# Kernel optimization log

Hardware: AMD Instinct MI355X
Metric: run time of the kernel (lower is better)

Reference implementation:

```python
import jax, jax.numpy as jnp
import numpy as np

N, E, D, H, C, G, L = 100000, 1600000, 128, 4, 32, 4096, 3  # nodes, edges, h_dim, heads, head_dim, graphs, conv blocks


def setup_inputs() -> dict:
    key = jax.random.key(0)
    ks = jax.random.split(key, 24)
    s = 0.05
    w = lambda k, shape: jax.random.normal(k, shape, jnp.float32) * s
    inp = {
        "x": jax.random.normal(ks[0], (N, D), jnp.float32),
        "edge_index": jax.random.randint(ks[1], (2, E), 0, N),
        "batch": jnp.sort(jax.random.randint(ks[2], (N,), 0, G)),
        # input TransformerConv (in=D, out=C per head, H heads, beta=True)
        "in_Wq": w(ks[3], (D, D)), "in_bq": jnp.zeros((D,), jnp.float32),
        "in_Wk": w(ks[4], (D, D)), "in_bk": jnp.zeros((D,), jnp.float32),
        "in_Wv": w(ks[5], (D, D)), "in_bv": jnp.zeros((D,), jnp.float32),
        "in_Ws": w(ks[6], (D, D)), "in_bs": jnp.zeros((D,), jnp.float32),
        "in_Wbeta": w(ks[7], (3 * D,)),
        # stacked conv blocks (L of them, in=out=D)
        "blk_Wq": w(ks[8], (L, D, D)), "blk_bq": jnp.zeros((L, D), jnp.float32),
        "blk_Wk": w(ks[9], (L, D, D)), "blk_bk": jnp.zeros((L, D), jnp.float32),
        "blk_Wv": w(ks[10], (L, D, D)), "blk_bv": jnp.zeros((L, D), jnp.float32),
        "blk_Ws": w(ks[11], (L, D, D)), "blk_bs": jnp.zeros((L, D), jnp.float32),
        "blk_Wbeta": w(ks[12], (L, 3 * D)),
        # MLP head
        "W1": w(ks[13], (D, 64)), "b1": jnp.zeros((64,), jnp.float32),
        "W2": w(ks[14], (64, 32)), "b2": jnp.zeros((32,), jnp.float32),
        "W3": w(ks[15], (32, 1)), "b3": jnp.zeros((1,), jnp.float32),
    }
    return inp


def transformer_conv(x, src, dst, Wq, bq, Wk, bk, Wv, bv, Ws, bs, Wbeta):
    # PyG TransformerConv, concat=True, root_weight=True, beta=True, eval mode
    q = (x @ Wq + bq).reshape(N, H, C)
    k = (x @ Wk + bk).reshape(N, H, C)
    v = (x @ Wv + bv).reshape(N, H, C)
    # per-edge attention logits: message j=src -> i=dst
    alpha = jnp.einsum("ehc,ehc->eh", q[dst], k[src]) / jnp.sqrt(jnp.float32(C))  # [E,H]
    m = jax.ops.segment_max(alpha, dst, num_segments=N)
    m = jnp.where(jnp.isfinite(m), m, 0.0)
    e = jnp.exp(alpha - m[dst])
    denom = jax.ops.segment_sum(e, dst, num_segments=N)
    a = e / (denom[dst] + 1e-16)  # segment softmax over in-edges of dst
    msg = a[..., None] * v[src]  # [E,H,C]
    out = jax.ops.segment_sum(msg, dst, num_segments=N).reshape(N, H * C)
    x_r = x @ Ws + bs
    beta = jax.nn.sigmoid(jnp.concatenate([out, x_r, out - x_r], axis=-1) @ Wbeta)[:, None]
    return beta * x_r + (1.0 - beta) * out


def reference(x, edge_index, batch, in_Wq, in_bq, in_Wk, in_bk, in_Wv, in_bv,
              in_Ws, in_bs, in_Wbeta, blk_Wq, blk_bq, blk_Wk, blk_bk, blk_Wv,
              blk_bv, blk_Ws, blk_bs, blk_Wbeta, W1, b1, W2, b2, W3, b3):
    src, dst = edge_index[0], edge_index[1]
    h = jax.nn.relu(transformer_conv(x, src, dst, in_Wq, in_bq, in_Wk, in_bk,
                                     in_Wv, in_bv, in_Ws, in_bs, in_Wbeta))
    for l in range(L):  # dropout is identity in eval mode
        h = jax.nn.relu(transformer_conv(h, src, dst, blk_Wq[l], blk_bq[l],
                                         blk_Wk[l], blk_bk[l], blk_Wv[l], blk_bv[l],
                                         blk_Ws[l], blk_bs[l], blk_Wbeta[l]))
    # global mean pool over graphs
    sums = jax.ops.segment_sum(h, batch, num_segments=G)
    cnt = jax.ops.segment_sum(jnp.ones((N, 1), h.dtype), batch, num_segments=G)
    g = sums / jnp.maximum(cnt, 1.0)
    g = jax.nn.relu(g @ W1 + b1)
    g = jax.nn.relu(g @ W2 + b2)
    return jax.nn.sigmoid(g @ W3 + b3)
```

## Files before the change

### kernel.cpp

```cpp
#include <hip/hip_runtime.h>
#include <hip/hip_bf16.h>
#include <cstdint>

#define DH 128
#define NB 256
#define NBK 1024

typedef __attribute__((ext_vector_type(8))) short short8;
typedef __attribute__((ext_vector_type(4))) float floatx4;
typedef __attribute__((ext_vector_type(2))) float floatx2;

__device__ __forceinline__ float bflo(unsigned u) { return __uint_as_float(u << 16); }
__device__ __forceinline__ float bfhi(unsigned u) { return __uint_as_float(u & 0xffff0000u); }

__device__ __forceinline__ unsigned pk_bf16(float a, float b) {
  return ((unsigned)__bfloat16_as_ushort(__float2bfloat16(b)) << 16)
       | (unsigned)__bfloat16_as_ushort(__float2bfloat16(a));
}

template<int CTRL>
__device__ __forceinline__ float dpp_add(float x) {
  int y = __builtin_amdgcn_update_dpp(0, __float_as_int(x), CTRL, 0xf, 0xf, true);
  return x + __int_as_float(y);
}


__global__ void cvt_bf16(const float* __restrict__ x, __hip_bfloat16* __restrict__ o, int n) {
  int i = blockIdx.x * 256 + threadIdx.x;
  if (i < n) o[i] = __float2bfloat16(x[i]);
}


__global__ void scan1_kernel(const int* __restrict__ deg, int* __restrict__ off,
                             int* __restrict__ bsum, int n) {
  __shared__ int sh[256];
  int idx = blockIdx.x * 256 + threadIdx.x;
  int v = (idx < n) ? deg[idx] : 0;
  sh[threadIdx.x] = v;
  __syncthreads();
  for (int d = 1; d < 256; d <<= 1) {
    int x = (threadIdx.x >= (unsigned)d) ? sh[threadIdx.x - d] : 0;
    __syncthreads();
    sh[threadIdx.x] += x;
    __syncthreads();
  }
  if (idx < n) off[idx] = sh[threadIdx.x] - v;
  if (threadIdx.x == 255) bsum[blockIdx.x] = sh[255];
}

__global__ void scan2_kernel(int* __restrict__ bsum, int nb) {
  __shared__ int sh[512];
  int t = threadIdx.x;
  int v = (t < nb) ? bsum[t] : 0;
  sh[t] = v;
  __syncthreads();
  for (int d = 1; d < 512; d <<= 1) {
    int x = (t >= (unsigned)d) ? sh[t - d] : 0;
    __syncthreads();
    sh[t] += x;
    __syncthreads();
  }
  if (t < nb) bsum[t] = sh[t] - v;
}

__global__ void scan3_kernel(int* __restrict__ off, const int* __restrict__ bsum, int n) {
  int idx = blockIdx.x * 256 + threadIdx.x;
  if (idx < n) off[idx] += bsum[blockIdx.x];
}


__global__ __launch_bounds__(256)
void csr_p1(const int* __restrict__ dst, int* __restrict__ hist, int E, int chunk) {
  __shared__ int cnt[NBK];
  const int blk = blockIdx.x, tid = threadIdx.x;
  for (int c = tid; c < NBK; c += 256) cnt[c] = 0;
  __syncthreads();
  int base = blk * chunk;
  int end = base + chunk; if (end > E) end = E;
  for (int e = base + tid; e < end; e += 256) atomicAdd(&cnt[dst[e] >> 7], 1);
  __syncthreads();
  for (int c = tid; c < NBK; c += 256) hist[c * NB + blk] = cnt[c];
}


__global__ __launch_bounds__(256)
void csr_p2(int* __restrict__ hist, int* __restrict__ total) {
  int b = blockIdx.x * 4 + (threadIdx.x >> 6);
  int lane = threadIdx.x & 63;
  int4 v = *(int4*)&hist[b * NB + lane * 4];
  int s0 = v.x;
  int s1 = s0 + v.y;
  int s2 = s1 + v.z;
  int s3 = s2 + v.w;
  int t = s3;
  for (int d = 1; d < 64; d <<= 1) {
    int y = __shfl_up(t, d);
    if (lane >= d) t += y;
  }
  int excl = t - s3;
  int4 o;
  o.x = excl; o.y = excl + s0; o.z = excl + s1; o.w = excl + s2;
  *(int4*)&hist[b * NB + lane * 4] = o;
  if (lane == 63) total[b] = t;
}

__global__ __launch_bounds__(256)
void csr_p3(const int* __restrict__ src, const int* __restrict__ dst,
            const int* __restrict__ hist, const int* __restrict__ tstart,
            int* __restrict__ part, int E, int chunk) {
  __shared__ int cur[NBK];
  const int blk = blockIdx.x, tid = threadIdx.x;
  for (int c = tid; c < NBK; c += 256) cur[c] = hist[c * NB + blk] + tstart[c];
  __syncthreads();
  int base = blk * chunk;
  int end = base + chunk; if (end > E) end = E;
  for (int e = base + tid; e < end; e += 256) {
    int d = dst[e];
    int b = d >> 7;
    int pos = atomicAdd(&cur[b], 1);
    part[pos] = (src[e] << 7) | (d & 127);
  }
}

__global__ __launch_bounds__(256)
void csr_p4(const int* __restrict__ part, const int* __restrict__ tstart,
            const int* __restrict__ total, int* __restrict__ deg,
            int* __restrict__ off, int* __restrict__ csr, int Nn) {
  __shared__ int lcnt[128], lscan[128], lcur[128];
  const int b = blockIdx.x, tid = threadIdx.x;
  const int p0 = tstart[b];
  const int m = total[b];
  if (tid < 128) lcnt[tid] = 0;
  __syncthreads();
  for (int k = tid; k < m; k += 256) atomicAdd(&lcnt[part[p0 + k] & 127], 1);
  __syncthreads();
  if (tid < 128) lscan[tid] = lcnt[tid];
  __syncthreads();
  for (int d = 1; d < 128; d <<= 1) {
    int v = 0;
    if (tid < 128 && tid >= d) v = lscan[tid - d];
    __syncthreads();
    if (tid < 128) lscan[tid] += v;
    __syncthreads();
  }
  if (tid < 128) {
    int ex = lscan[tid] - lcnt[tid];
    lcur[tid] = ex;
    int n = (b << 7) + tid;
    if (n < Nn) { deg[n] = lcnt[tid]; off[n] = p0 + ex; }
  }
  __syncthreads();
  for (int k = tid; k < m; k += 256) {
    int pk = part[p0 + k];
    int pos = p0 + atomicAdd(&lcur[pk & 127], 1);
    csr[pos] = pk >> 7;
  }
}


__global__ void goff_kernel(const int* __restrict__ batch, int* __restrict__ goff,
                            int N, int G) {
  int g = blockIdx.x * 256 + threadIdx.x;
  if (g > G) return;
  if (g == G) { goff[G] = N; return; }
  int lo = 0, hi = N;
  while (lo < hi) { int mid = (lo + hi) >> 1; if (batch[mid] < g) lo = mid + 1; else hi = mid; }
  goff[g] = lo;
}


__global__ __launch_bounds__(256)
void pack_w_kernel(const float* __restrict__ Wq, const float* __restrict__ Wk,
                   const float* __restrict__ Wv, const float* __restrict__ Ws,
                   const float* __restrict__ bq, const float* __restrict__ bk,
                   const float* __restrict__ bv, const float* __restrict__ bs,
                   __hip_bfloat16* __restrict__ WT2, float* __restrict__ bcat) {
  if (blockIdx.x == 64) {
    for (int c = threadIdx.x; c < 512; c += 256) {
      int which = c >> 7, cc = c & 127;
      const float* b = (which == 0) ? bq : (which == 1) ? bk : (which == 2) ? bv : bs;
      bcat[c] = b[cc];
    }
    return;
  }
  __shared__ float tile[32][33];
  const int bid = blockIdx.x;
  const int which = bid >> 4, kb = (bid >> 2) & 3, cb = bid & 3;
  const float* W = (which == 0) ? Wq : (which == 1) ? Wk : (which == 2) ? Wv : Ws;
  const int tx = threadIdx.x & 31, ty = threadIdx.x >> 5;
#pragma unroll
  for (int r = ty; r < 32; r += 8)
    tile[r][tx] = W[(kb * 32 + r) * 128 + cb * 32 + tx];
  __syncthreads();
  const int t = threadIdx.x;
  const int mt_sel = t >> 7;
  const int s4 = (t & 127) * 4;
  const int l16 = s4 >> 5;
  const int quad = (s4 >> 3) & 3;
  const int j0 = s4 & 7;
  const int cl = mt_sel * 16 + l16;
  const int kr = quad * 8 + j0;
  float f0 = tile[kr + 0][cl];
  float f1 = tile[kr + 1][cl];
  float f2 = tile[kr + 2][cl];
  float f3 = tile[kr + 3][cl];
  const int mt = which * 8 + cb * 2 + mt_sel;
  const int o = mt * 2048 + kb * 512 + l16 * 32 + quad * 8 + j0;
  uint2 w;
  w.x = pk_bf16(f0, f1);
  w.y = pk_bf16(f2, f3);
  *(uint2*)&((unsigned short*)WT2)[o] = w;
}


__global__ __launch_bounds__(256)
void gemm_qkvs(const short* __restrict__ Xb, const short* __restrict__ WT2,
               const float* __restrict__ bc,
               unsigned int* __restrict__ qout,
               unsigned int* __restrict__ kvp,
               unsigned int* __restrict__ xrout, int Nn) {
  __shared__ short As[64][132];
  const int row0 = blockIdx.x * 64;
  const int tid = threadIdx.x;

#pragma unroll
  for (int p = 0; p < 4; ++p) {
    int chunk = p * 256 + tid;
    int r = chunk >> 4, c8 = chunk & 15;
    int row = row0 + r; if (row >= Nn) row = Nn - 1;
    *(int4*)&As[r][c8 * 8] = *(const int4*)&Xb[(size_t)row * 128 + c8 * 8];
  }
  __syncthreads();

  const int w = tid >> 6, lane = tid & 63, quad = lane >> 4, l16 = lane & 15;

  short8 xf[4][4];
#pragma unroll
  for (int nt = 0; nt < 4; ++nt)
#pragma unroll
    for (int kt = 0; kt < 4; ++kt)
      xf[nt][kt] = *(const short8*)&As[nt * 16 + l16][kt * 32 + quad * 8];

  const int fbase = l16 * 32 + quad * 8;

  if (w == 0 || w == 3) {
    unsigned int* outp = (w == 0) ? qout : xrout;
    const int mbase = (w == 0) ? 0 : 24;
#pragma unroll
    for (int i = 0; i < 8; ++i) {
      const int mt = mbase + i;
      short8 af[4];
#pragma unroll
      for (int kt = 0; kt < 4; ++kt)
        af[kt] = *(const short8*)&WT2[mt * 2048 + kt * 512 + fbase];
      float4 bias = *(const float4*)&bc[mt * 16 + quad * 4];
      const int wc = (i * 16 + quad * 4);
#pragma unroll
      for (int nt = 0; nt < 4; ++nt) {
        floatx4 acc = (floatx4){0.f, 0.f, 0.f, 0.f};
#pragma unroll
        for (int kt = 0; kt < 4; ++kt)
          acc = __builtin_amdgcn_mfma_f32_16x16x32_bf16(af[kt], xf[nt][kt], acc, 0, 0, 0);
        int node = row0 + nt * 16 + l16;
        if (node < Nn) {
          uint2 o;
          o.x = pk_bf16(acc[0] + bias.x, acc[1] + bias.y);
          o.y = pk_bf16(acc[2] + bias.z, acc[3] + bias.w);
          *(uint2*)&outp[(size_t)node * 64 + (wc >> 1)] = o;
        }
      }
    }
  } else {
    const int kb = 8 + (w - 1) * 4;
    const int vb = 16 + (w - 1) * 4;
#pragma unroll
    for (int i = 0; i < 4; ++i) {
      const int mk = kb + i, mv = vb + i;
      short8 afk[4], afv[4];
#pragma unroll
      for (int kt = 0; kt < 4; ++kt) {
        afk[kt] = *(const short8*)&WT2[mk * 2048 + kt * 512 + fbase];
        afv[kt] = *(const short8*)&WT2[mv * 2048 + kt * 512 + fbase];
      }
      float4 bk4 = *(const float4*)&bc[mk * 16 + quad * 4];
      float4 bv4 = *(const float4*)&bc[mv * 16 + quad * 4];
      const int krel = (w - 1) * 64 + i * 16 + quad * 4;
#pragma unroll
      for (int nt = 0; nt < 4; ++nt) {
        floatx4 ak = (floatx4){0.f, 0.f, 0.f, 0.f};
        floatx4 av = (floatx4){0.f, 0.f, 0.f, 0.f};
#pragma unroll
        for (int kt = 0; kt < 4; ++kt) {
          ak = __builtin_amdgcn_mfma_f32_16x16x32_bf16(afk[kt], xf[nt][kt], ak, 0, 0, 0);
          av = __builtin_amdgcn_mfma_f32_16x16x32_bf16(afv[kt], xf[nt][kt], av, 0, 0, 0);
        }
        int node = row0 + nt * 16 + l16;
        if (node < Nn) {
          int d0 = __builtin_amdgcn_cvt_pk_fp8_f32(ak[0] + bk4.x, ak[1] + bk4.y, 0, false);
          d0 = __builtin_amdgcn_cvt_pk_fp8_f32(av[0] + bv4.x, av[1] + bv4.y, d0, true);
          int d1 = __builtin_amdgcn_cvt_pk_fp8_f32(ak[2] + bk4.z, ak[3] + bk4.w, 0, false);
          d1 = __builtin_amdgcn_cvt_pk_fp8_f32(av[2] + bv4.z, av[3] + bv4.w, d1, true);
          uint2 o; o.x = (unsigned)d0; o.y = (unsigned)d1;
          *(uint2*)&kvp[(size_t)node * 64 + (krel >> 1)] = o;
        }
      }
    }
  }
}


__global__ __launch_bounds__(256)
void attn_kernel(unsigned int* __restrict__ q_h, const unsigned int* __restrict__ kvp,
                 const unsigned int* __restrict__ xrb, const int* __restrict__ off,
                 const int* __restrict__ deg, const int* __restrict__ csr,
                 const float* __restrict__ Wb, int Nn) {
  int wv = __builtin_amdgcn_readfirstlane(threadIdx.x >> 6);
  int i = blockIdx.x * 4 + wv;
  if (i >= Nn) return;
  int l = threadIdx.x & 63;

  unsigned qp = q_h[(size_t)i * 64 + l];
  float q0 = bflo(qp), q1 = bfhi(qp);
  int e0 = off[i], e1 = e0 + deg[i];

  float den0 = 0.f, x00 = 0.f, x10 = 0.f;
  float den1 = 0.f, x01 = 0.f, x11 = 0.f;
  float den2 = 0.f, x02 = 0.f, x12 = 0.f;
  float den3 = 0.f, x03 = 0.f, x13 = 0.f;

  auto body = [&](int e, float& den, float& a0, float& a1) {
    int s = csr[e];
    int kq = (int)kvp[(s << 6) | l];
    floatx2 kk = __builtin_amdgcn_cvt_pk_f32_fp8(kq, false);
    floatx2 vv = __builtin_amdgcn_cvt_pk_f32_fp8(kq, true);
    float d = q0 * kk.x + q1 * kk.y;
    d = dpp_add<0x128>(d);
    d = dpp_add<0x124>(d);
    d = dpp_add<0x122>(d);
    d = dpp_add<0x121>(d);
    float p = __expf(d * 0.17677669529663687f);
    den += p; a0 += p * vv.x; a1 += p * vv.y;
  };

  int e = e0;
  for (; e + 3 < e1; e += 4) {
    body(e + 0, den0, x00, x10);
    body(e + 1, den1, x01, x11);
    body(e + 2, den2, x02, x12);
    body(e + 3, den3, x03, x13);
  }
  for (; e < e1; ++e) body(e, den0, x00, x10);

  float denom = den0 + den1 + den2 + den3 + 1e-16f;
  float o0 = (x00 + x01 + x02 + x03) / denom;
  float o1 = (x10 + x11 + x12 + x13) / denom;

  unsigned xp = xrb[(size_t)i * 64 + l];
  float xr0 = bflo(xp), xr1 = bfhi(xp);

  float c = o0 * Wb[2 * l] + o1 * Wb[2 * l + 1]
          + xr0 * Wb[128 + 2 * l] + xr1 * Wb[128 + 2 * l + 1]
          + (o0 - xr0) * Wb[256 + 2 * l] + (o1 - xr1) * Wb[256 + 2 * l + 1];
  c += __shfl_xor(c, 1);
  c += __shfl_xor(c, 2);
  c += __shfl_xor(c, 4);
  c += __shfl_xor(c, 8);
  c += __shfl_xor(c, 16);
  c += __shfl_xor(c, 32);
  float beta = 1.f / (1.f + __expf(-c));
  float h0 = fmaxf(beta * xr0 + (1.f - beta) * o0, 0.f);
  float h1 = fmaxf(beta * xr1 + (1.f - beta) * o1, 0.f);
  q_h[(size_t)i * 64 + l] = pk_bf16(h0, h1);
}


__global__ __launch_bounds__(128)
void poolmlp_kernel(const unsigned short* __restrict__ h, const int* __restrict__ goff,
                    const float* __restrict__ W1, const float* __restrict__ b1,
                    const float* __restrict__ W2, const float* __restrict__ b2,
                    const float* __restrict__ W3, const float* __restrict__ b3,
                    float* __restrict__ out) {
  int g = blockIdx.x;
  int t = threadIdx.x;
  int n0 = goff[g], cnt = goff[g + 1] - n0;
  float s = 0.f;
  for (int n = n0; n < n0 + cnt; ++n) s += bflo(h[(size_t)n * 128 + t]);
  __shared__ float gv[128];
  __shared__ float t1[64];
  __shared__ float t2[32];
  gv[t] = s / fmaxf((float)cnt, 1.0f);
  __syncthreads();
  if (t < 64) {
    float a = b1[t];
    for (int k = 0; k < 128; ++k) a += gv[k] * W1[k * 64 + t];
    t1[t] = fmaxf(a, 0.f);
  }
  __syncthreads();
  if (t < 32) {
    float a = b2[t];
    for (int k = 0; k < 64; ++k) a += t1[k] * W2[k * 32 + t];
    t2[t] = fmaxf(a, 0.f);
  }
  __syncthreads();
  if (t == 0) {
    float a = b3[0];
    for (int k = 0; k < 32; ++k) a += t2[k] * W3[k];
    out[g] = 1.f / (1.f + __expf(-a));
  }
}


extern "C" void kernel_launch(void* const* d_in, const int* in_sizes, int n_in,
                              void* d_out, int out_size, void* d_ws, size_t ws_size,
                              hipStream_t stream) {
  const float* x = (const float*)d_in[0];
  const int* edge_index = (const int*)d_in[1];
  const int* batch = (const int*)d_in[2];
  const int N = in_sizes[0] / DH;
  const int E = in_sizes[1] / 2;
  const int G = out_size;
  const int* src = edge_index;
  const int* dst = edge_index + E;

  const float* in_Wq = (const float*)d_in[3];
  const float* in_bq = (const float*)d_in[4];
  const float* in_Wk = (const float*)d_in[5];
  const float* in_bk = (const float*)d_in[6];
  const float* in_Wv = (const float*)d_in[7];
  const float* in_bv = (const float*)d_in[8];
  const float* in_Ws = (const float*)d_in[9];
  const float* in_bs = (const float*)d_in[10];
  const float* in_Wbeta = (const float*)d_in[11];
  const float* blk_Wq = (const float*)d_in[12];
  const float* blk_bq = (const float*)d_in[13];
  const float* blk_Wk = (const float*)d_in[14];
  const float* blk_bk = (const float*)d_in[15];
  const float* blk_Wv = (const float*)d_in[16];
  const float* blk_bv = (const float*)d_in[17];
  const float* blk_Ws = (const float*)d_in[18];
  const float* blk_bs = (const float*)d_in[19];
  const float* blk_Wbeta = (const float*)d_in[20];

  char* p = (char*)d_ws;
  auto take = [&](size_t bytes) { char* r = p; p += (bytes + 255) & ~(size_t)255; return r; };
  __hip_bfloat16* h0 = (__hip_bfloat16*)take((size_t)N * DH * 2);
  __hip_bfloat16* h1 = (__hip_bfloat16*)take((size_t)N * DH * 2);
  unsigned char* kvp = (unsigned char*)take((size_t)N * 256);
  unsigned short* xr = (unsigned short*)take((size_t)N * DH * 2);
  __hip_bfloat16* WT2 = (__hip_bfloat16*)take((size_t)512 * DH * 2);
  float* bcat = (float*)take(512 * 4);
  int* deg    = (int*)take((size_t)N * 4);
  int* off    = (int*)take((size_t)N * 4);
  int* csr    = (int*)take((size_t)E * 4);
  int* part   = (int*)take((size_t)E * 4);
  int* hist   = (int*)take((size_t)NB * NBK * 4);
  int* total  = (int*)take(NBK * 4);
  int* tstart = (int*)take(NBK * 4);
  int* bsumP  = (int*)take(512 * 4);
  int* goff   = (int*)take((size_t)(G + 1) * 4);
  (void)n_in;
  if ((size_t)(p - (char*)d_ws) > ws_size) return;

  const int NBUCK = (N + 127) >> 7;
  const int chunk = (E + NB - 1) / NB;

  csr_p1<<<NB, 256, 0, stream>>>(dst, hist, E, chunk);
  csr_p2<<<NBK / 4, 256, 0, stream>>>(hist, total);
  scan1_kernel<<<NBK / 256, 256, 0, stream>>>(total, tstart, bsumP, NBK);
  scan2_kernel<<<1, 512, 0, stream>>>(bsumP, NBK / 256);
  scan3_kernel<<<NBK / 256, 256, 0, stream>>>(tstart, bsumP, NBK);
  csr_p3<<<NB, 256, 0, stream>>>(src, dst, hist, tstart, part, E, chunk);
  csr_p4<<<NBUCK, 256, 0, stream>>>(part, tstart, total, deg, off, csr, N);

  goff_kernel<<<(G + 256) / 256, 256, 0, stream>>>(batch, goff, N, G);

  cvt_bf16<<<(int)(((size_t)N * DH + 255) / 256), 256, 0, stream>>>(x, h0, N * DH);

  for (int l = 0; l < 4; ++l) {
    const float *Wq, *Wk, *Wv, *Ws, *bq, *bk, *bv, *bs, *Wb;
    if (l == 0) {
      Wq = in_Wq; Wk = in_Wk; Wv = in_Wv; Ws = in_Ws;
      bq = in_bq; bk = in_bk; bv = in_bv; bs = in_bs; Wb = in_Wbeta;
    } else {
      int m = l - 1;
      Wq = blk_Wq + (size_t)m * DH * DH; Wk = blk_Wk + (size_t)m * DH * DH;
      Wv = blk_Wv + (size_t)m * DH * DH; Ws = blk_Ws + (size_t)m * DH * DH;
      bq = blk_bq + (size_t)m * DH; bk = blk_bk + (size_t)m * DH;
      bv = blk_bv + (size_t)m * DH; bs = blk_bs + (size_t)m * DH;
      Wb = blk_Wbeta + (size_t)m * 3 * DH;
    }
    __hip_bfloat16* hin  = (l & 1) ? h1 : h0;
    __hip_bfloat16* qbuf = (l & 1) ? h0 : h1;
    pack_w_kernel<<<65, 256, 0, stream>>>(Wq, Wk, Wv, Ws, bq, bk, bv, bs, WT2, bcat);
    gemm_qkvs<<<(N + 63) / 64, 256, 0, stream>>>((const short*)hin, (const short*)WT2, bcat,
        (unsigned int*)qbuf, (unsigned int*)kvp, (unsigned int*)xr, N);
    attn_kernel<<<(N + 3) / 4, 256, 0, stream>>>((unsigned int*)qbuf, (const unsigned int*)kvp,
        (const unsigned int*)xr, off, deg, csr, Wb, N);
  }

  poolmlp_kernel<<<G, 128, 0, stream>>>((const unsigned short*)h0, goff,
      (const float*)d_in[21], (const float*)d_in[22],
      (const float*)d_in[23], (const float*)d_in[24],
      (const float*)d_in[25], (const float*)d_in[26],
      (float*)d_out);
}
```

Before: 738.4 us.

## Process two edges per wavefront with half-waves in attention kernel

Restructures the attention kernel so each half-wave (32 lanes) handles one edge, with each lane covering 4 channels via 8-byte loads, so one wavefront processes two edges per step. The head-dim reduction now needs fewer DPP/shuffle steps, and the two half-wave partial sums are merged with a cross-half shuffle at the end. The softmax scale is folded into q with log2e so exp2f can be used. This is meant to cut per-edge instruction and reduction overhead and widen memory accesses, at the cost of extra shuffles and odd-degree handling where the spare half-wave does wasted loads.

```diff
diff --git a/kernel.cpp b/kernel.cpp
--- a/kernel.cpp
+++ b/kernel.cpp
@@ -310,67 +310,112 @@
 
 
 __global__ __launch_bounds__(256)
-void attn_kernel(unsigned int* __restrict__ q_h, const unsigned int* __restrict__ kvp,
-                 const unsigned int* __restrict__ xrb, const int* __restrict__ off,
+void attn_kernel(unsigned int* __restrict__ q_h, const uint2* __restrict__ kvp2,
+                 const uint2* __restrict__ xr2, const int* __restrict__ off,
                  const int* __restrict__ deg, const int* __restrict__ csr,
                  const float* __restrict__ Wb, int Nn) {
   int wv = __builtin_amdgcn_readfirstlane(threadIdx.x >> 6);
   int i = blockIdx.x * 4 + wv;
   if (i >= Nn) return;
-  int l = threadIdx.x & 63;
-
-  unsigned qp = q_h[(size_t)i * 64 + l];
-  float q0 = bflo(qp), q1 = bfhi(qp);
-  int e0 = off[i], e1 = e0 + deg[i];
-
-  float den0 = 0.f, x00 = 0.f, x10 = 0.f;
-  float den1 = 0.f, x01 = 0.f, x11 = 0.f;
-  float den2 = 0.f, x02 = 0.f, x12 = 0.f;
-  float den3 = 0.f, x03 = 0.f, x13 = 0.f;
-
-  auto body = [&](int e, float& den, float& a0, float& a1) {
-    int s = csr[e];
-    int kq = (int)kvp[(s << 6) | l];
-    floatx2 kk = __builtin_amdgcn_cvt_pk_f32_fp8(kq, false);
-    floatx2 vv = __builtin_amdgcn_cvt_pk_f32_fp8(kq, true);
-    float d = q0 * kk.x + q1 * kk.y;
-    d = dpp_add<0x128>(d);
-    d = dpp_add<0x124>(d);
-    d = dpp_add<0x122>(d);
-    d = dpp_add<0x121>(d);
-    float p = __expf(d * 0.17677669529663687f);
-    den += p; a0 += p * vv.x; a1 += p * vv.y;
+  const int l = threadIdx.x & 63;
+  const int j = l & 31;
+  const int g = l >> 5;
+
+  const float QS = 0.17677669529663687f * 1.4426950408889634f;
+  uint2 qw = ((const uint2*)q_h)[(size_t)i * 32 + j];
+  float q0 = bflo(qw.x) * QS, q1 = bfhi(qw.x) * QS;
+  float q2 = bflo(qw.y) * QS, q3 = bfhi(qw.y) * QS;
+
+  const int e0 = off[i];
+  const int dg = deg[i];
+
+  float denA = 0.f, aA0 = 0.f, aA1 = 0.f, aA2 = 0.f, aA3 = 0.f;
+  float denB = 0.f, aB0 = 0.f, aB1 = 0.f, aB2 = 0.f, aB3 = 0.f;
+
+  auto pair = [&](int s0, int s1, float& den, float& a0, float& a1, float& a2, float& a3) {
+    int s = g ? s1 : s0;
+    uint2 kv = kvp2[(unsigned)((s << 5) | j)];
+    floatx2 k01 = __builtin_amdgcn_cvt_pk_f32_fp8((int)kv.x, false);
+    floatx2 v01 = __builtin_amdgcn_cvt_pk_f32_fp8((int)kv.x, true);
+    floatx2 k23 = __builtin_amdgcn_cvt_pk_f32_fp8((int)kv.y, false);
+    floatx2 v23 = __builtin_amdgcn_cvt_pk_f32_fp8((int)kv.y, true);
+    float d = q0 * k01.x + q1 * k01.y + q2 * k23.x + q3 * k23.y;
+    d = dpp_add<0xB1>(d);
+    d = dpp_add<0x4E>(d);
+    d += __shfl_xor(d, 4);
+    float p = exp2f(d);
+    den += p;
+    a0 += p * v01.x; a1 += p * v01.y; a2 += p * v23.x; a3 += p * v23.y;
   };
 
+  const int nPair = dg >> 1;
   int e = e0;
-  for (; e + 3 < e1; e += 4) {
-    body(e + 0, den0, x00, x10);
-    body(e + 1, den1, x01, x11);
-    body(e + 2, den2, x02, x12);
-    body(e + 3, den3, x03, x13);
-  }
-  for (; e < e1; ++e) body(e, den0, x00, x10);
-
-  float denom = den0 + den1 + den2 + den3 + 1e-16f;
-  float o0 = (x00 + x01 + x02 + x03) / denom;
-  float o1 = (x10 + x11 + x12 + x13) / denom;
-
-  unsigned xp = xrb[(size_t)i * 64 + l];
-  float xr0 = bflo(xp), xr1 = bfhi(xp);
-
-  float c = o0 * Wb[2 * l] + o1 * Wb[2 * l + 1]
-          + xr0 * Wb[128 + 2 * l] + xr1 * Wb[128 + 2 * l + 1]
-          + (o0 - xr0) * Wb[256 + 2 * l] + (o1 - xr1) * Wb[256 + 2 * l + 1];
+  int it = 0;
+  for (; it + 1 < nPair; it += 2) {
+    int s0 = csr[e], s1 = csr[e + 1], s2 = csr[e + 2], s3 = csr[e + 3];
+    pair(s0, s1, denA, aA0, aA1, aA2, aA3);
+    pair(s2, s3, denB, aB0, aB1, aB2, aB3);
+    e += 4;
+  }
+  if (it < nPair) {
+    int s0 = csr[e], s1 = csr[e + 1];
+    pair(s0, s1, denA, aA0, aA1, aA2, aA3);
+    e += 2;
+  }
+  if (dg & 1) {
+    int s0 = csr[e];
+    int s = s0;
+    uint2 kv = kvp2[(unsigned)((s << 5) | j)];
+    floatx2 k01 = __builtin_amdgcn_cvt_pk_f32_fp8((int)kv.x, false);
+    floatx2 v01 = __builtin_amdgcn_cvt_pk_f32_fp8((int)kv.x, true);
+    floatx2 k23 = __builtin_amdgcn_cvt_pk_f32_fp8((int)kv.y, false);
+    floatx2 v23 = __builtin_amdgcn_cvt_pk_f32_fp8((int)kv.y, true);
+    float d = q0 * k01.x + q1 * k01.y + q2 * k23.x + q3 * k23.y;
+    d = dpp_add<0xB1>(d);
+    d = dpp_add<0x4E>(d);
+    d += __shfl_xor(d, 4);
+    float p = (g == 0) ? exp2f(d) : 0.f;
+    denB += p;
+    aB0 += p * v01.x; aB1 += p * v01.y; aB2 += p * v23.x; aB3 += p * v23.y;
+  }
+
+  float den = denA + denB;
+  float a0 = aA0 + aB0, a1 = aA1 + aB1, a2 = aA2 + aB2, a3 = aA3 + aB3;
+  den += __shfl_xor(den, 32);
+  a0 += __shfl_xor(a0, 32);
+  a1 += __shfl_xor(a1, 32);
+  a2 += __shfl_xor(a2, 32);
+  a3 += __shfl_xor(a3, 32);
+  float inv = 1.f / (den + 1e-16f);
+  float o0 = a0 * inv, o1 = a1 * inv, o2 = a2 * inv, o3 = a3 * inv;
+
+  uint2 xw = xr2[(size_t)i * 32 + j];
+  float xr0 = bflo(xw.x), xr1 = bfhi(xw.x);
+  float xr2v = bflo(xw.y), xr3 = bfhi(xw.y);
+
+  float4 wo = *(const float4*)&Wb[4 * j];
+  float4 wx = *(const float4*)&Wb[128 + 4 * j];
+  float4 wd = *(const float4*)&Wb[256 + 4 * j];
+  float c = o0 * wo.x + o1 * wo.y + o2 * wo.z + o3 * wo.w
+          + xr0 * wx.x + xr1 * wx.y + xr2v * wx.z + xr3 * wx.w
+          + (o0 - xr0) * wd.x + (o1 - xr1) * wd.y + (o2 - xr2v) * wd.z + (o3 - xr3) * wd.w;
   c += __shfl_xor(c, 1);
   c += __shfl_xor(c, 2);
   c += __shfl_xor(c, 4);
   c += __shfl_xor(c, 8);
   c += __shfl_xor(c, 16);
-  c += __shfl_xor(c, 32);
   float beta = 1.f / (1.f + __expf(-c));
-  float h0 = fmaxf(beta * xr0 + (1.f - beta) * o0, 0.f);
-  float h1 = fmaxf(beta * xr1 + (1.f - beta) * o1, 0.f);
-  q_h[(size_t)i * 64 + l] = pk_bf16(h0, h1);
+
+  if (g == 0) {
+    float h0 = fmaxf(beta * xr0 + (1.f - beta) * o0, 0.f);
+    float h1 = fmaxf(beta * xr1 + (1.f - beta) * o1, 0.f);
+    float h2 = fmaxf(beta * xr2v + (1.f - beta) * o2, 0.f);
+    float h3 = fmaxf(beta * xr3 + (1.f - beta) * o3, 0.f);
+    uint2 hw;
+    hw.x = pk_bf16(h0, h1);
+    hw.y = pk_bf16(h2, h3);
+    ((uint2*)q_h)[(size_t)i * 32 + j] = hw;
+  }
 }
 
 
@@ -494,8 +539,8 @@
     pack_w_kernel<<<65, 256, 0, stream>>>(Wq, Wk, Wv, Ws, bq, bk, bv, bs, WT2, bcat);
     gemm_qkvs<<<(N + 63) / 64, 256, 0, stream>>>((const short*)hin, (const short*)WT2, bcat,
         (unsigned int*)qbuf, (unsigned int*)kvp, (unsigned int*)xr, N);
-    attn_kernel<<<(N + 3) / 4, 256, 0, stream>>>((unsigned int*)qbuf, (const unsigned int*)kvp,
-        (const unsigned int*)xr, off, deg, csr, Wb, N);
+    attn_kernel<<<(N + 3) / 4, 256, 0, stream>>>((unsigned int*)qbuf, (const uint2*)kvp,
+        (const uint2*)xr, off, deg, csr, Wb, N);
   }
 
   poolmlp_kernel<<<G, 128, 0, stream>>>((const unsigned short*)h0, goff,
```

Result: no change. 725.6 us (-1.7%).
